# Optimization experiments

Hardware: AMD Instinct MI355X
Metric: run time of the kernel (lower is better)

The kernel has to match this reference:

```python
import jax, jax.numpy as jnp
import numpy as np

NUM_EMBEDDINGS = 768
HEAD_SIZE = 64

def setup_inputs() -> dict:
    key = jax.random.key(0)
    kx, kq, kk, kv = jax.random.split(key, 4)
    B, T, E, H = 4, 2048, NUM_EMBEDDINGS, HEAD_SIZE
    x = jax.random.normal(kx, (B, T, E), dtype=jnp.float32)
    s = 1.0 / np.sqrt(E)
    Wq = jax.random.normal(kq, (E, H), dtype=jnp.float32) * s
    Wk = jax.random.normal(kk, (E, H), dtype=jnp.float32) * s
    Wv = jax.random.normal(kv, (E, H), dtype=jnp.float32) * s
    return {"x": x, "Wq": Wq, "Wk": Wk, "Wv": Wv}

def reference(x, Wq, Wk, Wv):
    # x: [B,T,E]; Wq/Wk/Wv: [E,H]
    q = x @ Wq  # [B,T,H]
    k = x @ Wk
    v = x @ Wv
    scores = jnp.einsum('bth,bsh->bts', q, k) * (k.shape[-1] ** -0.5)  # [B,T,T]
    T = scores.shape[-1]
    # torch.tril(ones, diagonal=-1).bool(): True strictly below diagonal (t > s)
    row = jnp.arange(T)[:, None]
    col = jnp.arange(T)[None, :]
    mask = row > col  # strictly lower triangle masked to -inf
    scores = jnp.where(mask, -jnp.inf, scores)
    attn = jax.nn.softmax(scores, axis=-1)
    return attn @ v  # [B,T,H]
```

## Files before the change

### kernel.cpp

```cpp
#include <hip/hip_runtime.h>
#include <hip/hip_bf16.h>

#define T_ 2048
#define E_ 768

typedef __attribute__((ext_vector_type(8))) __bf16 bf16x8;
typedef __attribute__((ext_vector_type(8))) unsigned short ushort8;
typedef __attribute__((ext_vector_type(4))) unsigned short ushort4v;
typedef __attribute__((ext_vector_type(4))) float floatx4;

static __device__ __forceinline__ unsigned short f2bf(float f) {
    union { float f; unsigned u; } v; v.f = f;
    unsigned u = v.u;
    u += 0x7FFFu + ((u >> 16) & 1u);
    return (unsigned short)(u >> 16);
}

__global__ __launch_bounds__(256) void prep_wT(const float* __restrict__ Wq,
                                               const float* __restrict__ Wk,
                                               const float* __restrict__ Wv,
                                               unsigned short* __restrict__ wT) {
    int w  = blockIdx.x / 12;
    int k0 = (blockIdx.x % 12) * 64;
    const float* W = (w == 0) ? Wq : (w == 1 ? Wk : Wv);
    __shared__ unsigned short sm[64][65];
    int tid = threadIdx.x;
    #pragma unroll
    for (int i = 0; i < 16; ++i) {
        int idx = tid + i * 256;
        int k = idx >> 6, n = idx & 63;
        sm[n][k] = f2bf(W[(size_t)(k0 + k) * 64 + n]);
    }
    __syncthreads();
    #pragma unroll
    for (int i = 0; i < 16; ++i) {
        int idx = tid + i * 256;
        int n = idx >> 6, k = idx & 63;
        wT[(size_t)w * (64 * 768) + (size_t)n * 768 + k0 + k] = sm[n][k];
    }
}

__global__ __launch_bounds__(512) void qkv_proj(const float* __restrict__ x,
                                                const unsigned short* __restrict__ wT,
                                                unsigned short* __restrict__ Qb,
                                                unsigned short* __restrict__ Kb,
                                                unsigned short* __restrict__ vT) {
    __shared__ unsigned short ws_[192][72];
    __shared__ unsigned short xs[32][72];

    int tid  = threadIdx.x;
    int lane = tid & 63, wv = tid >> 6;
    int lrow = lane & 15;
    int kh   = lane >> 4;
    int lk   = kh * 8;
    int th   = wv >> 2;
    int wn   = wv & 3;
    int t0   = blockIdx.x * 32;
    int n0   = wn * 48;

    int wr = tid >> 3;
    int wc = (tid & 7) * 8;
    int xr = tid >> 4;
    int xc = (tid & 15) * 4;

    floatx4 acc[3] = {};

    for (int k0 = 0; k0 < 768; k0 += 64) {
        #pragma unroll
        for (int c = 0; c < 3; ++c) {
            int rw = c * 64 + wr;
            *(ushort8*)&ws_[rw][wc] = *(const ushort8*)(wT + (size_t)rw * 768 + k0 + wc);
        }
        {
            float4 a = *(const float4*)(x + (size_t)(t0 + xr) * 768 + k0 + xc);
            ushort4v p;
            p[0] = f2bf(a.x); p[1] = f2bf(a.y); p[2] = f2bf(a.z); p[3] = f2bf(a.w);
            *(ushort4v*)&xs[xr][xc] = p;
        }
        __syncthreads();
        #pragma unroll
        for (int kc = 0; kc < 2; ++kc) {
            bf16x8 af = *(const bf16x8*)&xs[th * 16 + lrow][kc * 32 + lk];
            #pragma unroll
            for (int nf = 0; nf < 3; ++nf) {
                bf16x8 bfv = *(const bf16x8*)&ws_[n0 + nf * 16 + lrow][kc * 32 + lk];
                acc[nf] = __builtin_amdgcn_mfma_f32_16x16x32_bf16(af, bfv, acc[nf], 0, 0, 0);
            }
        }
        __syncthreads();
    }

    const float QS = 0.18033688011112042f;
    int mt = t0 + th * 16 + kh * 4;
    #pragma unroll
    for (int nf = 0; nf < 3; ++nf) {
        int nb   = n0 + nf * 16;
        int widx = nb >> 6;
        int col  = (nb & 63) + lrow;
        if (widx == 0) {
            #pragma unroll
            for (int rg = 0; rg < 4; ++rg)
                Qb[(size_t)(mt + rg) * 64 + col] = f2bf(acc[nf][rg] * QS);
        } else if (widx == 1) {
            #pragma unroll
            for (int rg = 0; rg < 4; ++rg)
                Kb[(size_t)(mt + rg) * 64 + col] = f2bf(acc[nf][rg]);
        } else {
            int b  = mt >> 11;
            int tl = mt & 2047;
            ushort4v pk;
            #pragma unroll
            for (int rg = 0; rg < 4; ++rg) pk[rg] = f2bf(acc[nf][rg]);
            *(ushort4v*)&vT[(size_t)(b * 64 + col) * T_ + tl] = pk;
        }
    }
}

__global__ __launch_bounds__(256) void attn_part(const unsigned short* __restrict__ Qb,
                                                 const unsigned short* __restrict__ Kb,
                                                 const unsigned short* __restrict__ vT,
                                                 float* __restrict__ mP,
                                                 float* __restrict__ lP,
                                                 float* __restrict__ oP) {
    int c  = blockIdx.x;
    int qt = blockIdx.y;
    int b  = blockIdx.z;
    int t0 = qt * 64;
    int sBeg = t0 + c * 128;
    if (sBeg >= T_) return;
    int nt = ((T_ - sBeg) >= 128) ? 2 : 1;

    __shared__ unsigned short ks[2][64][72];
    __shared__ unsigned short vts[2][64][72];
    __shared__ unsigned short ps[4][16][72];

    int tid  = threadIdx.x;
    int lane = tid & 63, wv = tid >> 6;
    int lrow = lane & 15;
    int lk   = (lane >> 4) * 8;
    int qrow4 = (lane >> 4) * 4;
    int sr = tid >> 2, sc = tid & 3;

    const ushort8* kp0 = (const ushort8*)(Kb + (size_t)(b * T_ + sBeg + sr) * 64 + sc * 16);
    const ushort8* vp0 = (const ushort8*)(vT + (size_t)(b * 64 + sr) * T_ + sBeg + sc * 16);
    ushort8 k00 = kp0[0], k01 = kp0[1];
    ushort8 v00 = vp0[0], v01 = vp0[1];
    ushort8 k10, k11, v10, v11;
    if (nt == 2) {
        const ushort8* kp1 = (const ushort8*)(Kb + (size_t)(b * T_ + sBeg + 64 + sr) * 64 + sc * 16);
        const ushort8* vp1 = (const ushort8*)(vT + (size_t)(b * 64 + sr) * T_ + sBeg + 64 + sc * 16);
        k10 = kp1[0]; k11 = kp1[1];
        v10 = vp1[0]; v11 = vp1[1];
    }
    bf16x8 qf[2];
    {
        const unsigned short* qp = Qb + (size_t)(b * T_ + t0 + wv * 16 + lrow) * 64 + lk;
        qf[0] = *(const bf16x8*)(qp);
        qf[1] = *(const bf16x8*)(qp + 32);
    }

    *(ushort8*)&ks[0][sr][sc * 16]      = k00;
    *(ushort8*)&ks[0][sr][sc * 16 + 8]  = k01;
    *(ushort8*)&vts[0][sr][sc * 16]     = v00;
    *(ushort8*)&vts[0][sr][sc * 16 + 8] = v01;
    if (nt == 2) {
        *(ushort8*)&ks[1][sr][sc * 16]      = k10;
        *(ushort8*)&ks[1][sr][sc * 16 + 8]  = k11;
        *(ushort8*)&vts[1][sr][sc * 16]     = v10;
        *(ushort8*)&vts[1][sr][sc * 16 + 8] = v11;
    }
    __syncthreads();

    float m_[4], l_[4];
    floatx4 of[4] = {};
    #pragma unroll
    for (int rg = 0; rg < 4; ++rg) { m_[rg] = -__builtin_inff(); l_[rg] = 0.f; }

    auto tilecomp = [&](int buf, bool domask) {
        floatx4 sf[4] = {};
        #pragma unroll
        for (int kc = 0; kc < 2; ++kc) {
            bf16x8 af = qf[kc];
            #pragma unroll
            for (int nf = 0; nf < 4; ++nf) {
                bf16x8 bfv = *(const bf16x8*)&ks[buf][nf * 16 + lrow][kc * 32 + lk];
                sf[nf] = __builtin_amdgcn_mfma_f32_16x16x32_bf16(af, bfv, sf[nf], 0, 0, 0);
            }
        }

        if (domask) {
            #pragma unroll
            for (int nf = 0; nf < 4; ++nf)
                #pragma unroll
                for (int rg = 0; rg < 4; ++rg) {
                    int sl = nf * 16 + lrow;
                    int ql = wv * 16 + qrow4 + rg;
                    if (sl < ql) sf[nf][rg] = -__builtin_inff();
                }
        }

        float alpha[4];
        #pragma unroll
        for (int rg = 0; rg < 4; ++rg) {
            float v = fmaxf(fmaxf(sf[0][rg], sf[1][rg]), fmaxf(sf[2][rg], sf[3][rg]));
            v = fmaxf(v, __shfl_xor(v, 1, 64));
            v = fmaxf(v, __shfl_xor(v, 2, 64));
            v = fmaxf(v, __shfl_xor(v, 4, 64));
            v = fmaxf(v, __shfl_xor(v, 8, 64));
            float mn = fmaxf(m_[rg], v);
            alpha[rg] = exp2f(m_[rg] - mn);
            m_[rg] = mn;
            l_[rg] *= alpha[rg];
        }

        #pragma unroll
        for (int nf = 0; nf < 4; ++nf)
            #pragma unroll
            for (int rg = 0; rg < 4; ++rg) {
                float p = exp2f(sf[nf][rg] - m_[rg]);
                l_[rg] += p;
                ps[wv][qrow4 + rg][nf * 16 + lrow] = f2bf(p);
            }

        #pragma unroll
        for (int hf = 0; hf < 4; ++hf)
            #pragma unroll
            for (int rg = 0; rg < 4; ++rg)
                of[hf][rg] *= alpha[rg];

        #pragma unroll
        for (int kc = 0; kc < 2; ++kc) {
            bf16x8 pa = *(const bf16x8*)&ps[wv][lrow][kc * 32 + lk];
            #pragma unroll
            for (int hf = 0; hf < 4; ++hf) {
                bf16x8 vbv = *(const bf16x8*)&vts[buf][hf * 16 + lrow][kc * 32 + lk];
                of[hf] = __builtin_amdgcn_mfma_f32_16x16x32_bf16(pa, vbv, of[hf], 0, 0, 0);
            }
        }
    };

    tilecomp(0, c == 0);
    if (nt == 2) tilecomp(1, false);

    int p = (b * 32 + qt) * 16 + c;
    #pragma unroll
    for (int rg = 0; rg < 4; ++rg) {
        float v = l_[rg];
        v += __shfl_xor(v, 1, 64);
        v += __shfl_xor(v, 2, 64);
        v += __shfl_xor(v, 4, 64);
        v += __shfl_xor(v, 8, 64);
        l_[rg] = v;
    }
    if (lrow == 0) {
        #pragma unroll
        for (int rg = 0; rg < 4; ++rg) {
            int row = wv * 16 + qrow4 + rg;
            mP[(size_t)p * 64 + row] = m_[rg];
            lP[(size_t)p * 64 + row] = l_[rg];
        }
    }
    #pragma unroll
    for (int hf = 0; hf < 4; ++hf)
        #pragma unroll
        for (int rg = 0; rg < 4; ++rg) {
            int row = wv * 16 + qrow4 + rg;
            oP[((size_t)p * 64 + row) * 64 + hf * 16 + lrow] = of[hf][rg];
        }
}

__global__ __launch_bounds__(256) void combine(const float* __restrict__ mP,
                                               const float* __restrict__ lP,
                                               const float* __restrict__ oP,
                                               float* __restrict__ out) {
    int bq = blockIdx.x >> 2;
    int rq = blockIdx.x & 3;
    int qt = bq & 31;
    int b  = bq >> 5;
    int nch = (2175 - 64 * qt) >> 7;

    int tid = threadIdx.x;
    int r   = rq * 16 + (tid >> 4);
    int cb  = (tid & 15) * 4;

    float M = -__builtin_inff();
    for (int cc = 0; cc < nch; ++cc)
        M = fmaxf(M, mP[(size_t)(bq * 16 + cc) * 64 + r]);

    float L = 0.f;
    float4 o = {0.f, 0.f, 0.f, 0.f};
    for (int cc = 0; cc < nch; ++cc) {
        size_t p = (size_t)(bq * 16 + cc);
        float w = exp2f(mP[p * 64 + r] - M);
        L += lP[p * 64 + r] * w;
        float4 ov = *(const float4*)&oP[(p * 64 + r) * 64 + cb];
        o.x += ov.x * w; o.y += ov.y * w; o.z += ov.z * w; o.w += ov.w * w;
    }
    float inv = 1.0f / L;
    float4 res = {o.x * inv, o.y * inv, o.z * inv, o.w * inv};
    *(float4*)&out[((size_t)(b * T_ + qt * 64 + r)) * 64 + cb] = res;
}

extern "C" void kernel_launch(void* const* d_in, const int* in_sizes, int n_in,
                              void* d_out, int out_size, void* d_ws, size_t ws_size,
                              hipStream_t stream) {
    const float* x  = (const float*)d_in[0];
    const float* Wq = (const float*)d_in[1];
    const float* Wk = (const float*)d_in[2];
    const float* Wv = (const float*)d_in[3];
    float* out = (float*)d_out;

    unsigned short* wT = (unsigned short*)d_ws;
    unsigned short* Qb = wT + 3 * 64 * 768;
    unsigned short* Kb = Qb + 8192 * 64;
    unsigned short* vT = Kb + 8192 * 64;
    float* mP = (float*)(vT + 4 * 64 * T_);
    float* lP = mP + 128 * 16 * 64;
    float* oP = lP + 128 * 16 * 64;

    prep_wT<<<36, 256, 0, stream>>>(Wq, Wk, Wv, wT);
    qkv_proj<<<256, 512, 0, stream>>>(x, wT, Qb, Kb, vT);
    attn_part<<<dim3(16, 32, 4), 256, 0, stream>>>(Qb, Kb, vT, mP, lP, oP);
    combine<<<512, 256, 0, stream>>>(mP, lP, oP, out);
}
```

Baseline: 51.49 us.

## Widen attention key chunks to 256 with prefetch and halve projection block rows

The attention partial kernel now handles up to four 64-key tiles per block instead of two, halving the partial count and the combine traffic. The third and fourth tiles are prefetched into registers while the first two are being computed. The projection kernel switches to 16-row, 256-thread blocks with twice as many blocks, to spread the work over more CUs. In exchange there are fewer attention blocks and so less parallelism, longer serial work per block, and more register pressure from the prefetch buffers.

```diff
diff --git a/kernel.cpp b/kernel.cpp
--- a/kernel.cpp
+++ b/kernel.cpp
@@ -40,23 +40,21 @@
     }
 }
 
-__global__ __launch_bounds__(512) void qkv_proj(const float* __restrict__ x,
+__global__ __launch_bounds__(256) void qkv_proj(const float* __restrict__ x,
                                                 const unsigned short* __restrict__ wT,
                                                 unsigned short* __restrict__ Qb,
                                                 unsigned short* __restrict__ Kb,
                                                 unsigned short* __restrict__ vT) {
     __shared__ unsigned short ws_[192][72];
-    __shared__ unsigned short xs[32][72];
+    __shared__ unsigned short xs[16][72];
 
     int tid  = threadIdx.x;
     int lane = tid & 63, wv = tid >> 6;
     int lrow = lane & 15;
     int kh   = lane >> 4;
     int lk   = kh * 8;
-    int th   = wv >> 2;
-    int wn   = wv & 3;
-    int t0   = blockIdx.x * 32;
-    int n0   = wn * 48;
+    int t0   = blockIdx.x * 16;
+    int n0   = wv * 48;
 
     int wr = tid >> 3;
     int wc = (tid & 7) * 8;
@@ -67,8 +65,8 @@
 
     for (int k0 = 0; k0 < 768; k0 += 64) {
         #pragma unroll
-        for (int c = 0; c < 3; ++c) {
-            int rw = c * 64 + wr;
+        for (int c = 0; c < 6; ++c) {
+            int rw = c * 32 + wr;
             *(ushort8*)&ws_[rw][wc] = *(const ushort8*)(wT + (size_t)rw * 768 + k0 + wc);
         }
         {
@@ -80,7 +78,7 @@
         __syncthreads();
         #pragma unroll
         for (int kc = 0; kc < 2; ++kc) {
-            bf16x8 af = *(const bf16x8*)&xs[th * 16 + lrow][kc * 32 + lk];
+            bf16x8 af = *(const bf16x8*)&xs[lrow][kc * 32 + lk];
             #pragma unroll
             for (int nf = 0; nf < 3; ++nf) {
                 bf16x8 bfv = *(const bf16x8*)&ws_[n0 + nf * 16 + lrow][kc * 32 + lk];
@@ -91,7 +89,7 @@
     }
 
     const float QS = 0.18033688011112042f;
-    int mt = t0 + th * 16 + kh * 4;
+    int mt = t0 + kh * 4;
     #pragma unroll
     for (int nf = 0; nf < 3; ++nf) {
         int nb   = n0 + nf * 16;
@@ -126,9 +124,11 @@
     int qt = blockIdx.y;
     int b  = blockIdx.z;
     int t0 = qt * 64;
-    int sBeg = t0 + c * 128;
+    int sBeg = t0 + c * 256;
     if (sBeg >= T_) return;
-    int nt = ((T_ - sBeg) >= 128) ? 2 : 1;
+    int nt = (T_ - sBeg) >> 6; if (nt > 4) nt = 4;
+    int p0 = (nt < 2) ? nt : 2;
+    int p1 = nt - p0;
 
     __shared__ unsigned short ks[2][64][72];
     __shared__ unsigned short vts[2][64][72];
@@ -141,16 +141,19 @@
     int qrow4 = (lane >> 4) * 4;
     int sr = tid >> 2, sc = tid & 3;
 
-    const ushort8* kp0 = (const ushort8*)(Kb + (size_t)(b * T_ + sBeg + sr) * 64 + sc * 16);
-    const ushort8* vp0 = (const ushort8*)(vT + (size_t)(b * 64 + sr) * T_ + sBeg + sc * 16);
-    ushort8 k00 = kp0[0], k01 = kp0[1];
-    ushort8 v00 = vp0[0], v01 = vp0[1];
-    ushort8 k10, k11, v10, v11;
-    if (nt == 2) {
-        const ushort8* kp1 = (const ushort8*)(Kb + (size_t)(b * T_ + sBeg + 64 + sr) * 64 + sc * 16);
-        const ushort8* vp1 = (const ushort8*)(vT + (size_t)(b * 64 + sr) * T_ + sBeg + 64 + sc * 16);
-        k10 = kp1[0]; k11 = kp1[1];
-        v10 = vp1[0]; v11 = vp1[1];
+    const size_t kRow = (size_t)(b * T_ + sBeg + sr) * 64 + sc * 16;
+    const size_t vRow = (size_t)(b * 64 + sr) * T_ + sBeg + sc * 16;
+
+    ushort8 k0a = *(const ushort8*)(Kb + kRow);
+    ushort8 k0b = *(const ushort8*)(Kb + kRow + 8);
+    ushort8 v0a = *(const ushort8*)(vT + vRow);
+    ushort8 v0b = *(const ushort8*)(vT + vRow + 8);
+    ushort8 k1a, k1b, v1a, v1b;
+    if (p0 == 2) {
+        k1a = *(const ushort8*)(Kb + kRow + 64 * 64);
+        k1b = *(const ushort8*)(Kb + kRow + 64 * 64 + 8);
+        v1a = *(const ushort8*)(vT + vRow + 64);
+        v1b = *(const ushort8*)(vT + vRow + 64 + 8);
     }
     bf16x8 qf[2];
     {
@@ -159,17 +162,31 @@
         qf[1] = *(const bf16x8*)(qp + 32);
     }
 
-    *(ushort8*)&ks[0][sr][sc * 16]      = k00;
-    *(ushort8*)&ks[0][sr][sc * 16 + 8]  = k01;
-    *(ushort8*)&vts[0][sr][sc * 16]     = v00;
-    *(ushort8*)&vts[0][sr][sc * 16 + 8] = v01;
-    if (nt == 2) {
-        *(ushort8*)&ks[1][sr][sc * 16]      = k10;
-        *(ushort8*)&ks[1][sr][sc * 16 + 8]  = k11;
-        *(ushort8*)&vts[1][sr][sc * 16]     = v10;
-        *(ushort8*)&vts[1][sr][sc * 16 + 8] = v11;
+    *(ushort8*)&ks[0][sr][sc * 16]      = k0a;
+    *(ushort8*)&ks[0][sr][sc * 16 + 8]  = k0b;
+    *(ushort8*)&vts[0][sr][sc * 16]     = v0a;
+    *(ushort8*)&vts[0][sr][sc * 16 + 8] = v0b;
+    if (p0 == 2) {
+        *(ushort8*)&ks[1][sr][sc * 16]      = k1a;
+        *(ushort8*)&ks[1][sr][sc * 16 + 8]  = k1b;
+        *(ushort8*)&vts[1][sr][sc * 16]     = v1a;
+        *(ushort8*)&vts[1][sr][sc * 16 + 8] = v1b;
     }
     __syncthreads();
+
+    ushort8 k2a, k2b, v2a, v2b, k3a, k3b, v3a, v3b;
+    if (p1 >= 1) {
+        k2a = *(const ushort8*)(Kb + kRow + 2 * 64 * 64);
+        k2b = *(const ushort8*)(Kb + kRow + 2 * 64 * 64 + 8);
+        v2a = *(const ushort8*)(vT + vRow + 128);
+        v2b = *(const ushort8*)(vT + vRow + 128 + 8);
+    }
+    if (p1 == 2) {
+        k3a = *(const ushort8*)(Kb + kRow + 3 * 64 * 64);
+        k3b = *(const ushort8*)(Kb + kRow + 3 * 64 * 64 + 8);
+        v3a = *(const ushort8*)(vT + vRow + 192);
+        v3b = *(const ushort8*)(vT + vRow + 192 + 8);
+    }
 
     float m_[4], l_[4];
     floatx4 of[4] = {};
@@ -240,9 +257,26 @@
     };
 
     tilecomp(0, c == 0);
-    if (nt == 2) tilecomp(1, false);
-
-    int p = (b * 32 + qt) * 16 + c;
+    if (p0 == 2) tilecomp(1, false);
+
+    if (p1 >= 1) {
+        __syncthreads();
+        *(ushort8*)&ks[0][sr][sc * 16]      = k2a;
+        *(ushort8*)&ks[0][sr][sc * 16 + 8]  = k2b;
+        *(ushort8*)&vts[0][sr][sc * 16]     = v2a;
+        *(ushort8*)&vts[0][sr][sc * 16 + 8] = v2b;
+        if (p1 == 2) {
+            *(ushort8*)&ks[1][sr][sc * 16]      = k3a;
+            *(ushort8*)&ks[1][sr][sc * 16 + 8]  = k3b;
+            *(ushort8*)&vts[1][sr][sc * 16]     = v3a;
+            *(ushort8*)&vts[1][sr][sc * 16 + 8] = v3b;
+        }
+        __syncthreads();
+        tilecomp(0, false);
+        if (p1 == 2) tilecomp(1, false);
+    }
+
+    int p = (b * 32 + qt) * 8 + c;
     #pragma unroll
     for (int rg = 0; rg < 4; ++rg) {
         float v = l_[rg];
@@ -277,7 +311,7 @@
     int rq = blockIdx.x & 3;
     int qt = bq & 31;
     int b  = bq >> 5;
-    int nch = (2175 - 64 * qt) >> 7;
+    int nch = (2303 - 64 * qt) >> 8;
 
     int tid = threadIdx.x;
     int r   = rq * 16 + (tid >> 4);
@@ -285,12 +319,12 @@
 
     float M = -__builtin_inff();
     for (int cc = 0; cc < nch; ++cc)
-        M = fmaxf(M, mP[(size_t)(bq * 16 + cc) * 64 + r]);
+        M = fmaxf(M, mP[(size_t)(bq * 8 + cc) * 64 + r]);
 
     float L = 0.f;
     float4 o = {0.f, 0.f, 0.f, 0.f};
     for (int cc = 0; cc < nch; ++cc) {
-        size_t p = (size_t)(bq * 16 + cc);
+        size_t p = (size_t)(bq * 8 + cc);
         float w = exp2f(mP[p * 64 + r] - M);
         L += lP[p * 64 + r] * w;
         float4 ov = *(const float4*)&oP[(p * 64 + r) * 64 + cb];
@@ -315,11 +349,11 @@
     unsigned short* Kb = Qb + 8192 * 64;
     unsigned short* vT = Kb + 8192 * 64;
     float* mP = (float*)(vT + 4 * 64 * T_);
-    float* lP = mP + 128 * 16 * 64;
-    float* oP = lP + 128 * 16 * 64;
+    float* lP = mP + 128 * 8 * 64;
+    float* oP = lP + 128 * 8 * 64;
 
     prep_wT<<<36, 256, 0, stream>>>(Wq, Wk, Wv, wT);
-    qkv_proj<<<256, 512, 0, stream>>>(x, wT, Qb, Kb, vT);
-    attn_part<<<dim3(16, 32, 4), 256, 0, stream>>>(Qb, Kb, vT, mP, lP, oP);
+    qkv_proj<<<512, 256, 0, stream>>>(x, wT, Qb, Kb, vT);
+    attn_part<<<dim3(8, 32, 4), 256, 0, stream>>>(Qb, Kb, vT, mP, lP, oP);
     combine<<<512, 256, 0, stream>>>(mP, lP, oP, out);
 }
```

After: 49.42 us. 1.04x faster.
